# Performance work log

Hardware: AMD Instinct MI355X
Metric: run time of the kernel (lower is better)

## Reference

```python
import jax, jax.numpy as jnp
import numpy as np

C = 1.0          # ball curvature magnitude (manifold.c)
EPS = 1e-5       # boundary projection epsilon
MIN_NORM = 1e-15

def _norm(x):
    return jnp.maximum(jnp.linalg.norm(x, axis=-1, keepdims=True), MIN_NORM)

def artanh(x):
    return jnp.arctanh(jnp.clip(x, -1.0 + 1e-7, 1.0 - 1e-7))

def proj(x, c=C):
    # clip points to the open Poincare ball of radius 1/sqrt(c)
    n = _norm(x)
    maxnorm = (1.0 - EPS) / jnp.sqrt(c)
    return jnp.where(n > maxnorm, x / n * maxnorm, x)

def logmap0(x, c=C):
    sc = jnp.sqrt(c)
    n = _norm(x)
    return artanh(sc * n) * x / (sc * n)

def expmap0(u, c=C):
    sc = jnp.sqrt(c)
    n = _norm(u)
    return jnp.tanh(sc * n) * u / (sc * n)

def gyro_add(x, y, c=C):
    # Mobius (gyrovector) addition
    x2 = jnp.sum(x * x, -1, keepdims=True)
    y2 = jnp.sum(y * y, -1, keepdims=True)
    xy = jnp.sum(x * y, -1, keepdims=True)
    num = (1.0 + 2.0 * c * xy + c * y2) * x + (1.0 - c * x2) * y
    den = 1.0 + 2.0 * c * xy + c * c * x2 * y2
    return num / jnp.maximum(den, MIN_NORM)

def gyro_matvec(W, x, c=C):
    # Mobius matrix-vector multiplication (pv_gyro_matvec)
    sc = jnp.sqrt(c)
    xn = _norm(x)
    mx = x @ W.T                       # [N, out]
    mxn = _norm(mx)
    res = jnp.tanh(mxn / xn * artanh(sc * xn)) * mx / (mxn * sc)
    zero = jnp.all(mx == 0.0, axis=-1, keepdims=True)
    return jnp.where(zero, jnp.zeros_like(res), res)

def hyp_linear(x, W, b, c=C):
    # CustomHyperbolicLinear (activation=None branch): mobius matvec + hyp bias gyro-add
    res = proj(gyro_matvec(W, x, c), c)
    hyp_bias = proj(expmap0(b[None, :], c), c)   # proj_tan0 is identity on the ball
    res = proj(gyro_add(res, hyp_bias, c), c)
    return res

def hyp_tanh_act(x, c=C):
    # CustomHyperbolicActivation(manifold, nn.Tanh()): tanh in tangent space at origin
    x = proj(x, c)
    t = jnp.tanh(logmap0(x, c))
    return proj(expmap0(t, c), c)


def setup_inputs() -> dict:
    key = jax.random.key(0)
    k0, k1, k2 = jax.random.split(key, 3)
    N, D, H = 32768, 1024, 1024
    x = proj(0.1 * jax.random.normal(k0, (N, D), dtype=jnp.float32))
    gain = float(np.sqrt(2.0))
    bound1 = gain * float(np.sqrt(6.0 / (D + H)))   # xavier_uniform with gain sqrt(2)
    W1 = jax.random.uniform(k1, (H, D), jnp.float32, -bound1, bound1)
    b1 = jnp.zeros((H,), jnp.float32)
    bound2 = gain * float(np.sqrt(6.0 / (H + H)))
    W2 = jax.random.uniform(k2, (H, H), jnp.float32, -bound2, bound2)
    b2 = jnp.zeros((H,), jnp.float32)
    return {"x": x, "W1": W1, "b1": b1, "W2": W2, "b2": b2}


def reference(x, W1, b1, W2, b2):
    # GeometricModel forward: two CustomHyperbolicLayer blocks
    # (hyperbolic linear -> tangent-space tanh activation)
    h = hyp_linear(x, W1, b1)
    h = hyp_tanh_act(h)
    h = hyp_linear(h, W2, b2)
    h = hyp_tanh_act(h)
    return h
```

## Files before the change

### kernel.cpp

```cpp
#include <hip/hip_runtime.h>


typedef short short8 __attribute__((ext_vector_type(8)));
typedef unsigned short u16x8 __attribute__((ext_vector_type(8)));
typedef unsigned short u16x4 __attribute__((ext_vector_type(4)));
typedef float f32x4 __attribute__((ext_vector_type(4)));

#define MAXN (1.0f - 1e-5f)

__device__ __forceinline__ float bf2f(unsigned short u) {
    return __uint_as_float(((unsigned int)u) << 16);
}
__device__ __forceinline__ unsigned short f2bf(float f) {
    unsigned int u = __float_as_uint(f);
    u += 0x7FFFu + ((u >> 16) & 1u);
    return (unsigned short)(u >> 16);
}
__device__ __forceinline__ float wave_sum(float v) {
#pragma unroll
    for (int m = 32; m > 0; m >>= 1) v += __shfl_xor(v, m, 64);
    return v;
}
__device__ __forceinline__ float artanh_clip(float x) {
    x = fminf(fmaxf(x, -1.0f + 1e-7f), 1.0f - 1e-7f);
    return 0.5f * logf((1.0f + x) / (1.0f - x));
}

__device__ __forceinline__ void gld_lds16(const unsigned short* g, unsigned short* l) {
    __builtin_amdgcn_global_load_lds(
        (const __attribute__((address_space(1))) unsigned int*)g,
        (__attribute__((address_space(3))) unsigned int*)l,
        16, 0, 0);
}

__global__ __launch_bounds__(256) void cast_x_kernel(
    const float* __restrict__ X, unsigned short* __restrict__ Xb,
    float* __restrict__ xn, int K)
{
    int row = blockIdx.x * 4 + (threadIdx.x >> 6);
    int l = threadIdx.x & 63;
    const float4* xr = (const float4*)(X + (size_t)row * K);
    u16x4* xw = (u16x4*)(Xb + (size_t)row * K);
    float ss = 0.f;
#pragma unroll
    for (int i = 0; i < 4; ++i) {
        float4 v = xr[i * 64 + l];
        ss += v.x * v.x + v.y * v.y + v.z * v.z + v.w * v.w;
        u16x4 o;
        o[0] = f2bf(v.x); o[1] = f2bf(v.y); o[2] = f2bf(v.z); o[3] = f2bf(v.w);
        xw[i * 64 + l] = o;
    }
    ss = wave_sum(ss);
    if (l == 0) xn[row] = fmaxf(sqrtf(ss), 1e-15f);
}

__global__ __launch_bounds__(256) void cast_w_kernel(
    const float* __restrict__ W, unsigned short* __restrict__ Wb, int n4)
{
    int i = blockIdx.x * 256 + threadIdx.x;
    if (i >= n4) return;
    float4 v = ((const float4*)W)[i];
    u16x4 o;
    o[0] = f2bf(v.x); o[1] = f2bf(v.y); o[2] = f2bf(v.z); o[3] = f2bf(v.w);
    ((u16x4*)Wb)[i] = o;
}

#define STAGE(rs_, kt_) do {                                            \
    const int ko_ = (kt_) << 5;                                         \
    gld_lds16(Ab + ga0 + ko_, &sA[(rs_) * 8192 + c0 * 8]);              \
    gld_lds16(Ab + ga1 + ko_, &sA[(rs_) * 8192 + c1 * 8]);              \
    gld_lds16(Bb + ga0 + ko_, &sB[(rs_) * 8192 + c0 * 8]);              \
    gld_lds16(Bb + ga1 + ko_, &sB[(rs_) * 8192 + c1 * 8]);              \
} while (0)

#define KSTEP(kt_, DOSTAGE_, VMSTR_, DOSYNC_) {                                     \
    if (DOSTAGE_) { STAGE(((kt_) + 3) & 3, (kt_) + 3); }                            \
    const int rb_ = ((kt_) & 3) * 8192;                                             \
    const unsigned short* pa_ = &sA[rb_ + (wm + lr) * 32 + swo];                    \
    const unsigned short* pb_ = &sB[rb_ + (wn + lr) * 32 + swo];                    \
    short8 av_[8]; short8 bv_[4];                                                   \
    _Pragma("unroll")                                                               \
    for (int m_ = 0; m_ < 8; ++m_) av_[m_] = *(const short8*)(pa_ + m_ * 512);      \
    _Pragma("unroll")                                                               \
    for (int n_ = 0; n_ < 4; ++n_) bv_[n_] = *(const short8*)(pb_ + n_ * 512);      \
    __builtin_amdgcn_s_setprio(1);                                                  \
    _Pragma("unroll")                                                               \
    for (int m_ = 0; m_ < 8; ++m_)                                                  \
        _Pragma("unroll")                                                           \
        for (int n_ = 0; n_ < 4; ++n_)                                              \
            acc[m_][n_] = __builtin_amdgcn_mfma_f32_16x16x32_bf16(                  \
                av_[m_], bv_[n_], acc[m_][n_], 0, 0, 0);                            \
    __builtin_amdgcn_s_setprio(0);                                                  \
    if (DOSYNC_) {                                                                  \
        asm volatile("s_waitcnt vmcnt(" VMSTR_ ")" ::: "memory");                   \
        __builtin_amdgcn_s_barrier();                                               \
    }                                                                               \
}

__global__ __launch_bounds__(512, 2) void gemm_bt_kernel(
    const unsigned short* __restrict__ A,
    const unsigned short* __restrict__ B,
    unsigned short* __restrict__ C,
    int M, int Nc, int K)
{
    __shared__ __align__(16) unsigned short sA[4 * 256 * 32];
    __shared__ __align__(16) unsigned short sB[4 * 256 * 32];

    const int t = threadIdx.x;
    const int l = t & 63;
    const int w = t >> 6;
    const int lr = l & 15;
    const int lq = l >> 4;

    const int nwg = gridDim.x;
    const int cpx = nwg >> 3;
    const int swz = (blockIdx.x & 7) * cpx + (blockIdx.x >> 3);
    const int nb = Nc >> 8;
    const int bm = swz / nb;
    const int bn = swz % nb;

    const unsigned short* Ab = A + (size_t)bm * 256 * K;
    const unsigned short* Bb = B + (size_t)bn * 256 * K;

    const int wm = (w >> 2) * 128;
    const int wn = (w & 3) * 64;

    const int c0 = t, c1 = t + 512;
    const int r0 = c0 >> 2, s0 = (c0 & 3) ^ ((r0 >> 1) & 3);
    const int r1 = c1 >> 2, s1 = (c1 & 3) ^ ((r1 >> 1) & 3);
    const size_t ga0 = (size_t)r0 * K + s0 * 8;
    const size_t ga1 = (size_t)r1 * K + s1 * 8;

    const int swo = (lq ^ ((lr >> 1) & 3)) * 8;

    f32x4 acc[8][4];
#pragma unroll
    for (int i = 0; i < 8; ++i)
#pragma unroll
        for (int j = 0; j < 4; ++j)
            acc[i][j] = (f32x4){0.f, 0.f, 0.f, 0.f};

    STAGE(0, 0);
    STAGE(1, 1);
    STAGE(2, 2);
    asm volatile("s_waitcnt vmcnt(8)" ::: "memory");
    __builtin_amdgcn_s_barrier();

    const int NTK = K >> 5;
    int kt = 0;
#pragma unroll 1
    for (; kt < NTK - 3; ++kt) {
        KSTEP(kt, true, "8", true);
    }
    KSTEP(kt, false, "4", true); ++kt;
    KSTEP(kt, false, "0", true); ++kt;
    KSTEP(kt, false, "0", false);

    unsigned short* Cb = C + (size_t)(bm * 256 + wm) * Nc + bn * 256 + wn;
#pragma unroll
    for (int i = 0; i < 8; ++i)
#pragma unroll
        for (int r = 0; r < 4; ++r) {
            unsigned short* Cr = Cb + (size_t)(i * 16 + lq * 4 + r) * Nc + lr;
#pragma unroll
            for (int j = 0; j < 4; ++j)
                Cr[j * 16] = f2bf(acc[i][j][r]);
        }
}

template <int OUTF32>
__global__ __launch_bounds__(256) void hyp_epilogue_kernel(
    const unsigned short* __restrict__ mx, const float* __restrict__ xn_in,
    const float* __restrict__ bvec, void* __restrict__ outp,
    float* __restrict__ xn_out, int H)
{
    int row = blockIdx.x * 4 + (threadIdx.x >> 6);
    int l = threadIdx.x & 63;
    const u16x8* mrow = (const u16x8*)(mx + (size_t)row * H);
    u16x8 mv0 = mrow[l], mv1 = mrow[64 + l];
    const float4* bf4 = (const float4*)bvec;
    float4 bq0 = bf4[l * 2], bq1 = bf4[l * 2 + 1];
    float4 bq2 = bf4[128 + l * 2], bq3 = bf4[128 + l * 2 + 1];

    float m[16], b[16];
#pragma unroll
    for (int i = 0; i < 8; ++i) { m[i] = bf2f(mv0[i]); m[8 + i] = bf2f(mv1[i]); }
    b[0] = bq0.x; b[1] = bq0.y; b[2] = bq0.z; b[3] = bq0.w;
    b[4] = bq1.x; b[5] = bq1.y; b[6] = bq1.z; b[7] = bq1.w;
    b[8] = bq2.x; b[9] = bq2.y; b[10] = bq2.z; b[11] = bq2.w;
    b[12] = bq3.x; b[13] = bq3.y; b[14] = bq3.z; b[15] = bq3.w;

    float ssm = 0.f, ssb = 0.f, dmb = 0.f;
#pragma unroll
    for (int i = 0; i < 16; ++i) {
        ssm += m[i] * m[i]; ssb += b[i] * b[i]; dmb += m[i] * b[i];
    }
    ssm = wave_sum(ssm); ssb = wave_sum(ssb); dmb = wave_sum(dmb);

    float mxn = fmaxf(sqrtf(ssm), 1e-15f);
    float bn  = fmaxf(sqrtf(ssb), 1e-15f);
    float xn  = xn_in[row];

    float tt = tanhf(mxn / xn * artanh_clip(xn));
    float rnorm = fabsf(tt);
    float pr = (rnorm > MAXN) ? (MAXN / rnorm) : 1.0f;
    float resScale = tt * pr / mxn;
    float rn = fminf(rnorm, MAXN);
    float x2 = rn * rn;

    float tb = tanhf(bn);
    float hbn = fabsf(tb);
    float pb = (hbn > MAXN) ? (MAXN / hbn) : 1.0f;
    float hscale = (tb / bn) * pb;
    float hn = fminf(hbn, MAXN);
    float y2 = hn * hn;

    float xy = resScale * hscale * dmb;
    float ca = 1.0f + 2.0f * xy + y2;
    float cb = 1.0f - x2;
    float den = fmaxf(1.0f + 2.0f * xy + x2 * y2, 1e-15f);
    float fA = ca * resScale / den;
    float fB = cb * hscale / den;

    float ssz = fA * fA * ssm + 2.0f * fA * fB * dmb + fB * fB * ssb;
    float zn = fmaxf(sqrtf(fmaxf(ssz, 0.0f)), 1e-15f);
    float pz = (zn > MAXN) ? (MAXN / zn) : 1.0f;
    float n2 = fmaxf(fminf(zn, MAXN), 1e-15f);
    float g = (artanh_clip(n2) / n2) * pz;

    float u[16];
    float ssu = 0.f;
#pragma unroll
    for (int i = 0; i < 16; ++i) {
        float zi = fA * m[i] + fB * b[i];
        u[i] = tanhf(g * zi);
        ssu += u[i] * u[i];
    }
    ssu = wave_sum(ssu);
    float un = fmaxf(sqrtf(ssu), 1e-15f);
    float te = tanhf(un);
    float on = fabsf(te);
    float po = (on > MAXN) ? (MAXN / on) : 1.0f;
    float os = (te / un) * po;

    if (OUTF32) {
        float* of = (float*)outp + (size_t)row * H;
        float4* of4 = (float4*)of;
        float4 a0, a1, a2, a3;
        a0.x = os * u[0];  a0.y = os * u[1];  a0.z = os * u[2];  a0.w = os * u[3];
        a1.x = os * u[4];  a1.y = os * u[5];  a1.z = os * u[6];  a1.w = os * u[7];
        a2.x = os * u[8];  a2.y = os * u[9];  a2.z = os * u[10]; a2.w = os * u[11];
        a3.x = os * u[12]; a3.y = os * u[13]; a3.z = os * u[14]; a3.w = os * u[15];
        of4[l * 2] = a0; of4[l * 2 + 1] = a1;
        of4[128 + l * 2] = a2; of4[128 + l * 2 + 1] = a3;
    } else {
        u16x8 o0, o1;
#pragma unroll
        for (int i = 0; i < 8; ++i) { o0[i] = f2bf(os * u[i]); o1[i] = f2bf(os * u[8 + i]); }
        u16x8* orow = (u16x8*)((unsigned short*)outp + (size_t)row * H);
        orow[l] = o0; orow[64 + l] = o1;
    }
    if (l == 0) xn_out[row] = fmaxf(fminf(on, MAXN), 1e-15f);
}

extern "C" void kernel_launch(void* const* d_in, const int* in_sizes, int n_in,
                              void* d_out, int out_size, void* d_ws, size_t ws_size,
                              hipStream_t stream)
{
    const float* x  = (const float*)d_in[0];
    const float* W1 = (const float*)d_in[1];
    const float* b1 = (const float*)d_in[2];
    const float* W2 = (const float*)d_in[3];
    const float* b2 = (const float*)d_in[4];

    const int H = in_sizes[2];
    const int D = in_sizes[1] / H;
    const int N = in_sizes[0] / D;

    unsigned short* stage = (unsigned short*)d_out;
    float* outf = (float*)d_out;

    unsigned short* mxb = (unsigned short*)d_ws;
    unsigned short* W1b = mxb + (size_t)N * H;
    unsigned short* W2b = W1b + (size_t)H * D;
    float* xn1 = (float*)(W2b + (size_t)H * H);
    float* xn2 = xn1 + N;

    dim3 blk(256);
    dim3 gblk(512);
    const int gemm_grid = (N / 256) * (H / 256);

    cast_x_kernel<<<N / 4, blk, 0, stream>>>(x, stage, xn1, D);
    cast_w_kernel<<<(H * D / 4 + 255) / 256, blk, 0, stream>>>(W1, W1b, H * D / 4);
    cast_w_kernel<<<(H * H / 4 + 255) / 256, blk, 0, stream>>>(W2, W2b, H * H / 4);
    gemm_bt_kernel<<<gemm_grid, gblk, 0, stream>>>(stage, W1b, mxb, N, H, D);
    hyp_epilogue_kernel<0><<<N / 4, blk, 0, stream>>>(mxb, xn1, b1, stage, xn2, H);
    gemm_bt_kernel<<<gemm_grid, gblk, 0, stream>>>(stage, W2b, mxb, N, H, H);
    hyp_epilogue_kernel<1><<<N / 4, blk, 0, stream>>>(mxb, xn2, b2, outf, xn1, H);
}
```

Measured before the change: 468.8 us.

## Split GEMM k-step into two half-phases interleaving LDS reads, global prefetch, and MFMA

Each k-step of the bf16 GEMM main loop becomes two phases. Each phase loads half of the A fragments from LDS, issues half of the global-to-LDS prefetch for a later stage (A in the first phase, B in the second), synchronises with barriers, then runs 16 MFMAs. The aim is to spread memory traffic between MFMA bursts so loads and compute overlap better and fewer fragment registers are live at once, at the cost of extra barriers per k-step. The two weight-cast kernels are also merged into a single launch.

```diff
diff --git a/kernel.cpp b/kernel.cpp
--- a/kernel.cpp
+++ b/kernel.cpp
@@ -55,14 +55,18 @@
 }
 
 __global__ __launch_bounds__(256) void cast_w_kernel(
-    const float* __restrict__ W, unsigned short* __restrict__ Wb, int n4)
+    const float* __restrict__ W1, unsigned short* __restrict__ W1b,
+    const float* __restrict__ W2, unsigned short* __restrict__ W2b, int n4each)
 {
     int i = blockIdx.x * 256 + threadIdx.x;
-    if (i >= n4) return;
-    float4 v = ((const float4*)W)[i];
+    const float4* src;
+    u16x4* dst;
+    if (i < n4each) { src = (const float4*)W1; dst = (u16x4*)W1b; }
+    else            { src = (const float4*)W2; dst = (u16x4*)W2b; i -= n4each; }
+    float4 v = src[i];
     u16x4 o;
     o[0] = f2bf(v.x); o[1] = f2bf(v.y); o[2] = f2bf(v.z); o[3] = f2bf(v.w);
-    ((u16x4*)Wb)[i] = o;
+    dst[i] = o;
 }
 
 #define STAGE(rs_, kt_) do {                                            \
@@ -73,28 +77,55 @@
     gld_lds16(Bb + ga1 + ko_, &sB[(rs_) * 8192 + c1 * 8]);              \
 } while (0)
 
-#define KSTEP(kt_, DOSTAGE_, VMSTR_, DOSYNC_) {                                     \
-    if (DOSTAGE_) { STAGE(((kt_) + 3) & 3, (kt_) + 3); }                            \
+#define KSTEP(kt_, DOSTAGE_, DOVM_, VMSTR_, DOEND_) {                               \
     const int rb_ = ((kt_) & 3) * 8192;                                             \
     const unsigned short* pa_ = &sA[rb_ + (wm + lr) * 32 + swo];                    \
     const unsigned short* pb_ = &sB[rb_ + (wn + lr) * 32 + swo];                    \
-    short8 av_[8]; short8 bv_[4];                                                   \
-    _Pragma("unroll")                                                               \
-    for (int m_ = 0; m_ < 8; ++m_) av_[m_] = *(const short8*)(pa_ + m_ * 512);      \
+                     \
+    short8 bv_[4], av_[4];                                                          \
     _Pragma("unroll")                                                               \
     for (int n_ = 0; n_ < 4; ++n_) bv_[n_] = *(const short8*)(pb_ + n_ * 512);      \
+    _Pragma("unroll")                                                               \
+    for (int m_ = 0; m_ < 4; ++m_) av_[m_] = *(const short8*)(pa_ + m_ * 512);      \
+    if (DOSTAGE_) {                                                                 \
+        const int ko_ = ((kt_) + 3) << 5;                                           \
+        const int rs_ = (((kt_) + 3) & 3) * 8192;                                   \
+        gld_lds16(Ab + ga0 + ko_, &sA[rs_ + c0 * 8]);                               \
+        gld_lds16(Ab + ga1 + ko_, &sA[rs_ + c1 * 8]);                               \
+    }                                                                               \
+    __builtin_amdgcn_s_barrier();                                                   \
+    asm volatile("s_waitcnt lgkmcnt(0)" ::: "memory");                              \
     __builtin_amdgcn_s_setprio(1);                                                  \
     _Pragma("unroll")                                                               \
-    for (int m_ = 0; m_ < 8; ++m_)                                                  \
+    for (int m_ = 0; m_ < 4; ++m_)                                                  \
         _Pragma("unroll")                                                           \
         for (int n_ = 0; n_ < 4; ++n_)                                              \
             acc[m_][n_] = __builtin_amdgcn_mfma_f32_16x16x32_bf16(                  \
                 av_[m_], bv_[n_], acc[m_][n_], 0, 0, 0);                            \
     __builtin_amdgcn_s_setprio(0);                                                  \
-    if (DOSYNC_) {                                                                  \
-        asm volatile("s_waitcnt vmcnt(" VMSTR_ ")" ::: "memory");                   \
-        __builtin_amdgcn_s_barrier();                                               \
+    __builtin_amdgcn_s_barrier();                                                   \
+                             \
+    short8 aw_[4];                                                                  \
+    _Pragma("unroll")                                                               \
+    for (int m_ = 0; m_ < 4; ++m_) aw_[m_] = *(const short8*)(pa_ + (m_ + 4) * 512);\
+    if (DOSTAGE_) {                                                                 \
+        const int ko_ = ((kt_) + 3) << 5;                                           \
+        const int rs_ = (((kt_) + 3) & 3) * 8192;                                   \
+        gld_lds16(Bb + ga0 + ko_, &sB[rs_ + c0 * 8]);                               \
+        gld_lds16(Bb + ga1 + ko_, &sB[rs_ + c1 * 8]);                               \
     }                                                                               \
+    __builtin_amdgcn_s_barrier();                                                   \
+    asm volatile("s_waitcnt lgkmcnt(0)" ::: "memory");                              \
+    __builtin_amdgcn_s_setprio(1);                                                  \
+    _Pragma("unroll")                                                               \
+    for (int m_ = 0; m_ < 4; ++m_)                                                  \
+        _Pragma("unroll")                                                           \
+        for (int n_ = 0; n_ < 4; ++n_)                                              \
+            acc[m_ + 4][n_] = __builtin_amdgcn_mfma_f32_16x16x32_bf16(              \
+                aw_[m_], bv_[n_], acc[m_ + 4][n_], 0, 0, 0);                        \
+    __builtin_amdgcn_s_setprio(0);                                                  \
+    if (DOVM_) { asm volatile("s_waitcnt vmcnt(" VMSTR_ ")" ::: "memory"); }        \
+    if (DOEND_) { __builtin_amdgcn_s_barrier(); }                                   \
 }
 
 __global__ __launch_bounds__(512, 2) void gemm_bt_kernel(
@@ -150,11 +181,11 @@
     int kt = 0;
 #pragma unroll 1
     for (; kt < NTK - 3; ++kt) {
-        KSTEP(kt, true, "8", true);
-    }
-    KSTEP(kt, false, "4", true); ++kt;
-    KSTEP(kt, false, "0", true); ++kt;
-    KSTEP(kt, false, "0", false);
+        KSTEP(kt, true, true, "8", true);
+    }
+    KSTEP(kt, false, true, "4", true); ++kt;
+    KSTEP(kt, false, true, "0", true); ++kt;
+    KSTEP(kt, false, false, "0", false);
 
     unsigned short* Cb = C + (size_t)(bm * 256 + wm) * Nc + bn * 256 + wn;
 #pragma unroll
@@ -289,10 +320,10 @@
     dim3 blk(256);
     dim3 gblk(512);
     const int gemm_grid = (N / 256) * (H / 256);
+    const int n4w = H * D / 4;
 
     cast_x_kernel<<<N / 4, blk, 0, stream>>>(x, stage, xn1, D);
-    cast_w_kernel<<<(H * D / 4 + 255) / 256, blk, 0, stream>>>(W1, W1b, H * D / 4);
-    cast_w_kernel<<<(H * H / 4 + 255) / 256, blk, 0, stream>>>(W2, W2b, H * H / 4);
+    cast_w_kernel<<<(2 * n4w + 255) / 256, blk, 0, stream>>>(W1, W1b, W2, W2b, n4w);
     gemm_bt_kernel<<<gemm_grid, gblk, 0, stream>>>(stage, W1b, mxb, N, H, D);
     hyp_epilogue_kernel<0><<<N / 4, blk, 0, stream>>>(mxb, xn1, b1, stage, xn2, H);
     gemm_bt_kernel<<<gemm_grid, gblk, 0, stream>>>(stage, W2b, mxb, N, H, H);
```

After: 470.1 us. About the same (+0.3%).

## Double-buffer LDS fragments in registers across k-steps and fuse weight casts

Applied to the files above, without the earlier changes.

The GEMM main loop now loads the next k-tile's A/B fragments from LDS into a second register set while the MFMAs for the current tile run. This is meant to hide LDS read latency behind matrix-core work. The vmcnt waits are tightened so the tile being prefetched has already landed, and the loop is unrolled by two to alternate the register buffers. The two weight-cast launches are also merged into one, saving a launch. The extra 96 fragment registers raise register pressure under launch_bounds(512,2), which risks spills or lower occupancy.

```diff
diff --git a/kernel.cpp b/kernel.cpp
--- a/kernel.cpp
+++ b/kernel.cpp
@@ -55,14 +55,18 @@
 }
 
 __global__ __launch_bounds__(256) void cast_w_kernel(
-    const float* __restrict__ W, unsigned short* __restrict__ Wb, int n4)
+    const float* __restrict__ W1, unsigned short* __restrict__ W1b,
+    const float* __restrict__ W2, unsigned short* __restrict__ W2b, int n4each)
 {
     int i = blockIdx.x * 256 + threadIdx.x;
-    if (i >= n4) return;
-    float4 v = ((const float4*)W)[i];
+    const float4* src;
+    u16x4* dst;
+    if (i < n4each) { src = (const float4*)W1; dst = (u16x4*)W1b; }
+    else            { src = (const float4*)W2; dst = (u16x4*)W2b; i -= n4each; }
+    float4 v = src[i];
     u16x4 o;
     o[0] = f2bf(v.x); o[1] = f2bf(v.y); o[2] = f2bf(v.z); o[3] = f2bf(v.w);
-    ((u16x4*)Wb)[i] = o;
+    dst[i] = o;
 }
 
 #define STAGE(rs_, kt_) do {                                            \
@@ -73,28 +77,32 @@
     gld_lds16(Bb + ga1 + ko_, &sB[(rs_) * 8192 + c1 * 8]);              \
 } while (0)
 
-#define KSTEP(kt_, DOSTAGE_, VMSTR_, DOSYNC_) {                                     \
-    if (DOSTAGE_) { STAGE(((kt_) + 3) & 3, (kt_) + 3); }                            \
+#define LDFRAG(FA_, FB_, kt_) do {                                                  \
     const int rb_ = ((kt_) & 3) * 8192;                                             \
     const unsigned short* pa_ = &sA[rb_ + (wm + lr) * 32 + swo];                    \
     const unsigned short* pb_ = &sB[rb_ + (wn + lr) * 32 + swo];                    \
-    short8 av_[8]; short8 bv_[4];                                                   \
     _Pragma("unroll")                                                               \
-    for (int m_ = 0; m_ < 8; ++m_) av_[m_] = *(const short8*)(pa_ + m_ * 512);      \
+    for (int m_ = 0; m_ < 8; ++m_) FA_[m_] = *(const short8*)(pa_ + m_ * 512);      \
     _Pragma("unroll")                                                               \
-    for (int n_ = 0; n_ < 4; ++n_) bv_[n_] = *(const short8*)(pb_ + n_ * 512);      \
-    __builtin_amdgcn_s_setprio(1);                                                  \
+    for (int n_ = 0; n_ < 4; ++n_) FB_[n_] = *(const short8*)(pb_ + n_ * 512);      \
+} while (0)
+
+#define MFMAB(FA_, FB_)                                                             \
     _Pragma("unroll")                                                               \
     for (int m_ = 0; m_ < 8; ++m_)                                                  \
         _Pragma("unroll")                                                           \
         for (int n_ = 0; n_ < 4; ++n_)                                              \
             acc[m_][n_] = __builtin_amdgcn_mfma_f32_16x16x32_bf16(                  \
-                av_[m_], bv_[n_], acc[m_][n_], 0, 0, 0);                            \
+                FA_[m_], FB_[n_], acc[m_][n_], 0, 0, 0);
+
+#define PSTEP(kt_, FAC_, FBC_, FAN_, FBN_, DOSTAGE_, DOPF_, DOVM_, VMSTR_, DOBAR_) {\
+    if (DOSTAGE_) { STAGE((((kt_) + 3) & 3), (kt_) + 3); }                          \
+    if (DOPF_) { LDFRAG(FAN_, FBN_, (kt_) + 1); }                                   \
+    __builtin_amdgcn_s_setprio(1);                                                  \
+    MFMAB(FAC_, FBC_);                                                              \
     __builtin_amdgcn_s_setprio(0);                                                  \
-    if (DOSYNC_) {                                                                  \
-        asm volatile("s_waitcnt vmcnt(" VMSTR_ ")" ::: "memory");                   \
-        __builtin_amdgcn_s_barrier();                                               \
-    }                                                                               \
+    if (DOVM_) { asm volatile("s_waitcnt vmcnt(" VMSTR_ ")" ::: "memory"); }        \
+    if (DOBAR_) { __builtin_amdgcn_s_barrier(); }                                   \
 }
 
 __global__ __launch_bounds__(512, 2) void gemm_bt_kernel(
@@ -143,18 +151,23 @@
     STAGE(0, 0);
     STAGE(1, 1);
     STAGE(2, 2);
-    asm volatile("s_waitcnt vmcnt(8)" ::: "memory");
+    asm volatile("s_waitcnt vmcnt(4)" ::: "memory");
     __builtin_amdgcn_s_barrier();
+
+    short8 fa0[8], fb0[4], fa1[8], fb1[4];
+    LDFRAG(fa0, fb0, 0);
 
     const int NTK = K >> 5;
     int kt = 0;
 #pragma unroll 1
-    for (; kt < NTK - 3; ++kt) {
-        KSTEP(kt, true, "8", true);
-    }
-    KSTEP(kt, false, "4", true); ++kt;
-    KSTEP(kt, false, "0", true); ++kt;
-    KSTEP(kt, false, "0", false);
+    for (; kt < NTK - 4; kt += 2) {
+        PSTEP(kt,     fa0, fb0, fa1, fb1, true, true, true, "4", true);
+        PSTEP(kt + 1, fa1, fb1, fa0, fb0, true, true, true, "4", true);
+    }
+    PSTEP(NTK - 4, fa0, fb0, fa1, fb1, true,  true,  true,  "4", true);
+    PSTEP(NTK - 3, fa1, fb1, fa0, fb0, false, true,  true,  "0", true);
+    PSTEP(NTK - 2, fa0, fb0, fa1, fb1, false, true,  false, "0", false);
+    PSTEP(NTK - 1, fa1, fb1, fa0, fb0, false, false, false, "0", false);
 
     unsigned short* Cb = C + (size_t)(bm * 256 + wm) * Nc + bn * 256 + wn;
 #pragma unroll
@@ -289,10 +302,10 @@
     dim3 blk(256);
     dim3 gblk(512);
     const int gemm_grid = (N / 256) * (H / 256);
+    const int n4w = H * D / 4;
 
     cast_x_kernel<<<N / 4, blk, 0, stream>>>(x, stage, xn1, D);
-    cast_w_kernel<<<(H * D / 4 + 255) / 256, blk, 0, stream>>>(W1, W1b, H * D / 4);
-    cast_w_kernel<<<(H * H / 4 + 255) / 256, blk, 0, stream>>>(W2, W2b, H * H / 4);
+    cast_w_kernel<<<(2 * n4w + 255) / 256, blk, 0, stream>>>(W1, W1b, W2, W2b, n4w);
     gemm_bt_kernel<<<gemm_grid, gblk, 0, stream>>>(stage, W1b, mxb, N, H, D);
     hyp_epilogue_kernel<0><<<N / 4, blk, 0, stream>>>(mxb, xn1, b1, stage, xn2, H);
     gemm_bt_kernel<<<gemm_grid, gblk, 0, stream>>>(stage, W2b, mxb, N, H, H);
```

Measured after the change: 457.0 us. 1.03x faster.
